# Kernel tuning notes

Hardware: AMD Instinct MI355X
Metric: run time of the kernel (lower is better)

The kernel has to match this reference:

```python
import jax, jax.numpy as jnp
import numpy as np

N = 100000
EPS_BN = 1e-5


def setup_inputs() -> dict:
    key = jax.random.key(0)
    ks = jax.random.split(key, 12)
    x = jax.random.normal(ks[0], (N, 128), dtype=jnp.float32)
    edge_index = jax.random.randint(ks[1], (2, 800000), 0, N, dtype=jnp.int64)
    # GCNConv layer params (PyG: lin weight [out,in], bias added after aggregation)
    s = 1.0 / np.sqrt(128.0)
    W1 = jax.random.uniform(ks[2], (128, 128), jnp.float32, -s, s)
    b1 = jnp.zeros((128,), jnp.float32)
    W2 = jax.random.uniform(ks[3], (128, 128), jnp.float32, -s, s)
    b2 = jnp.zeros((128,), jnp.float32)
    # BatchNorm affine params
    g1 = jnp.ones((128,), jnp.float32)
    be1 = jnp.zeros((128,), jnp.float32)
    g2 = jnp.ones((128,), jnp.float32)
    be2 = jnp.zeros((128,), jnp.float32)
    # PReLU single shared parameter (torch init = 0.25)
    a = jnp.asarray(0.25, jnp.float32)
    return {"x": x, "edge_index": edge_index, "W1": W1, "b1": b1, "g1": g1,
            "be1": be1, "W2": W2, "b2": b2, "g2": g2, "be2": be2, "a": a}


def _gcn_conv(x, src, dst, deg_inv_sqrt, W, b):
    # x' = D^-1/2 (A+I) D^-1/2 (x W^T) + b  (self loops already in src/dst)
    h = x @ W.T                                   # [N, out]
    norm = deg_inv_sqrt[src] * deg_inv_sqrt[dst]  # [E+N]
    msg = h[src] * norm[:, None]                  # gather + scale
    out = jax.ops.segment_sum(msg, dst, num_segments=N)  # scatter-add
    return out + b


def _batchnorm(x, g, be):
    # training-mode BatchNorm1d over nodes (biased variance)
    mean = jnp.mean(x, axis=0)
    var = jnp.mean(jnp.square(x - mean), axis=0)
    return (x - mean) * jax.lax.rsqrt(var + EPS_BN) * g + be


def _prelu(x, a):
    return jnp.where(x > 0, x, a * x)


def reference(x, edge_index, W1, b1, g1, be1, W2, b2, g2, be2, a):
    # add self loops
    loops = jnp.arange(N, dtype=edge_index.dtype)
    src = jnp.concatenate([edge_index[0], loops])
    dst = jnp.concatenate([edge_index[1], loops])
    # symmetric normalization from in-degree at destinations
    deg = jax.ops.segment_sum(jnp.ones_like(dst, dtype=x.dtype), dst, num_segments=N)
    deg_inv_sqrt = jnp.where(deg > 0, jax.lax.rsqrt(deg), 0.0)

    h = _gcn_conv(x, src, dst, deg_inv_sqrt, W1, b1)
    h = _prelu(_batchnorm(h, g1, be1), a)
    h = _gcn_conv(h, src, dst, deg_inv_sqrt, W2, b2)
    h = _prelu(_batchnorm(h, g2, be2), a)
    return h
```

## Files before the change

kernel.cpp:

```cpp
#include <hip/hip_runtime.h>
#include <cstddef>
#include <cstdint>


#define EPS_BN 1e-5f
#define BN_BLOCKS 256

typedef short short8 __attribute__((ext_vector_type(8)));
typedef float f32x4 __attribute__((ext_vector_type(4)));

static __device__ __forceinline__ unsigned short f2b(float f) {
    union { float f; uint32_t u; } v; v.f = f;
    uint32_t u = v.u;
    return (unsigned short)((u + 0x7FFFu + ((u >> 16) & 1u)) >> 16);
}
static __device__ __forceinline__ float b2f(unsigned short h) {
    union { uint32_t u; float f; } v; v.u = ((uint32_t)h) << 16;
    return v.f;
}
static __device__ __forceinline__ float b2f_s(short h) { return b2f((unsigned short)h); }

__global__ __launch_bounds__(256) void k_count(const int* __restrict__ dst, int* __restrict__ cnt,
                                               int* __restrict__ rank, int E) {
    int e = blockIdx.x * 256 + threadIdx.x;
    if (e < E) rank[e] = atomicAdd(&cnt[dst[e]], 1);
}

__global__ __launch_bounds__(256) void k_scanA(const int* __restrict__ cnt, int* __restrict__ partial, int n) {
    __shared__ int sd[256];
    int tid = threadIdx.x;
    int base = blockIdx.x * 1024 + tid * 4;
    int s = 0;
#pragma unroll
    for (int j = 0; j < 4; j++) { int idx = base + j; if (idx < n) s += cnt[idx]; }
    sd[tid] = s; __syncthreads();
    for (int off = 128; off > 0; off >>= 1) {
        if (tid < off) sd[tid] += sd[tid + off];
        __syncthreads();
    }
    if (tid == 0) partial[blockIdx.x] = sd[0];
}

__global__ __launch_bounds__(128) void k_scanB(int* partial, int nb) {
    __shared__ int sd[128];
    int t = threadIdx.x;
    sd[t] = (t < nb) ? partial[t] : 0;
    __syncthreads();
    for (int off = 1; off < 128; off <<= 1) {
        int v = (t >= off) ? sd[t - off] : 0;
        __syncthreads();
        sd[t] += v;
        __syncthreads();
    }
    if (t < nb) partial[t] = (t == 0) ? 0 : sd[t - 1];
}

__global__ __launch_bounds__(256) void k_scanC(const int* __restrict__ cnt, const int* __restrict__ partial,
                                               int* __restrict__ rowptr, float* __restrict__ dis, int n) {
    __shared__ int sd[256];
    int tid = threadIdx.x;
    int base = blockIdx.x * 1024 + tid * 4;
    int v[4]; int s = 0;
#pragma unroll
    for (int j = 0; j < 4; j++) { int idx = base + j; v[j] = (idx < n) ? cnt[idx] : 0; s += v[j]; }
    sd[tid] = s; __syncthreads();
    for (int off = 1; off < 256; off <<= 1) {
        int u = (tid >= off) ? sd[tid - off] : 0;
        __syncthreads();
        sd[tid] += u;
        __syncthreads();
    }
    int excl = partial[blockIdx.x] + ((tid == 0) ? 0 : sd[tid - 1]);
#pragma unroll
    for (int j = 0; j < 4; j++) {
        int idx = base + j;
        if (idx < n) {
            rowptr[idx] = excl;
            dis[idx] = rsqrtf((float)(v[j] + 1));
        }
        excl += v[j];
    }
}

__global__ __launch_bounds__(256) void k_fill(const int* __restrict__ src, const int* __restrict__ dst,
                                              const int* __restrict__ rowptr, const int* __restrict__ rank,
                                              int* __restrict__ colw, int E) {
    int e = blockIdx.x * 256 + threadIdx.x;
    if (e < E) {
        int d = dst[e];
        colw[rowptr[d] + rank[e]] = src[e];
    }
}

__global__ __launch_bounds__(256) void k_wprep(const float* __restrict__ W1, const float* __restrict__ W2,
                                               unsigned short* __restrict__ Wz1, unsigned short* __restrict__ Wz2) {
    int gi = blockIdx.x * 256 + threadIdx.x;
    const float* W = (gi < 16384) ? W1 : W2;
    unsigned short* Wz = (gi < 16384) ? Wz1 : Wz2;
    int idx = gi & 16383;
    int o = idx >> 7, k = idx & 127;
    int ct = o >> 4, nn = o & 15, ks = k >> 5, q = (k >> 3) & 3, j = k & 7;
    Wz[(ct * 4 + ks) * 512 + (q * 16 + nn) * 8 + j] = f2b(W[idx]);
}

__global__ __launch_bounds__(256) void k_gemm1(const float* __restrict__ X,
                                               const unsigned short* __restrict__ Wz,
                                               unsigned short* __restrict__ Yb, int n) {
    __shared__ unsigned short lds[16384];
    int tid = threadIdx.x;
    const short8* wsrc = (const short8*)Wz;
    short8* ldst = (short8*)lds;
#pragma unroll
    for (int i = 0; i < 8; i++) ldst[tid + 256 * i] = wsrc[tid + 256 * i];
    __syncthreads();

    int wave = tid >> 6, lane = tid & 63;
    int r0 = blockIdx.x * 64 + wave * 16;
    int mrow = lane & 15, quad = lane >> 4;
    int arow = r0 + mrow; if (arow > n - 1) arow = n - 1;
    const float* xr = X + (size_t)arow * 128;

    f32x4 acc[8];
#pragma unroll
    for (int ct = 0; ct < 8; ct++) acc[ct] = (f32x4){0.f, 0.f, 0.f, 0.f};

#pragma unroll
    for (int ks = 0; ks < 4; ks++) {
        int kb = ks * 32 + quad * 8;
        float4 x0 = *reinterpret_cast<const float4*>(xr + kb);
        float4 x1 = *reinterpret_cast<const float4*>(xr + kb + 4);
        short8 a;
        a[0] = (short)f2b(x0.x); a[1] = (short)f2b(x0.y); a[2] = (short)f2b(x0.z); a[3] = (short)f2b(x0.w);
        a[4] = (short)f2b(x1.x); a[5] = (short)f2b(x1.y); a[6] = (short)f2b(x1.z); a[7] = (short)f2b(x1.w);
#pragma unroll
        for (int ct = 0; ct < 8; ct++) {
            short8 b = *(const short8*)(lds + (ct * 4 + ks) * 512 + lane * 8);
            acc[ct] = __builtin_amdgcn_mfma_f32_16x16x32_bf16(a, b, acc[ct], 0, 0, 0);
        }
    }
#pragma unroll
    for (int i = 0; i < 4; i++) {
        int row = r0 + quad * 4 + i;
        if (row < n) {
#pragma unroll
            for (int ct = 0; ct < 8; ct++)
                Yb[(size_t)row * 128 + ct * 16 + mrow] = f2b(acc[ct][i]);
        }
    }
}

__global__ __launch_bounds__(256) void k_gemm2(const unsigned short* __restrict__ Ab,
                                               const unsigned short* __restrict__ Wz,
                                               const float* __restrict__ sc, const float* __restrict__ sh,
                                               const float* __restrict__ ap,
                                               unsigned short* __restrict__ Yb, int n) {
    __shared__ unsigned short lds[16384];
    int tid = threadIdx.x;
    const short8* wsrc = (const short8*)Wz;
    short8* ldst = (short8*)lds;
#pragma unroll
    for (int i = 0; i < 8; i++) ldst[tid + 256 * i] = wsrc[tid + 256 * i];
    __syncthreads();

    float alpha = ap[0];
    int wave = tid >> 6, lane = tid & 63;
    int r0 = blockIdx.x * 64 + wave * 16;
    int mrow = lane & 15, quad = lane >> 4;
    int arow = r0 + mrow; if (arow > n - 1) arow = n - 1;
    const unsigned short* ar = Ab + (size_t)arow * 128;

    f32x4 acc[8];
#pragma unroll
    for (int ct = 0; ct < 8; ct++) acc[ct] = (f32x4){0.f, 0.f, 0.f, 0.f};

#pragma unroll
    for (int ks = 0; ks < 4; ks++) {
        int kb = ks * 32 + quad * 8;
        short8 raw = *(const short8*)(ar + kb);
        float4 s0 = *reinterpret_cast<const float4*>(sc + kb);
        float4 s1 = *reinterpret_cast<const float4*>(sc + kb + 4);
        float4 t0 = *reinterpret_cast<const float4*>(sh + kb);
        float4 t1 = *reinterpret_cast<const float4*>(sh + kb + 4);
        float ss[8] = {s0.x, s0.y, s0.z, s0.w, s1.x, s1.y, s1.z, s1.w};
        float tt[8] = {t0.x, t0.y, t0.z, t0.w, t1.x, t1.y, t1.z, t1.w};
        short8 a;
#pragma unroll
        for (int j = 0; j < 8; j++) {
            float x = fmaf(b2f_s(raw[j]), ss[j], tt[j]);
            x = x > 0.f ? x : alpha * x;
            a[j] = (short)f2b(x);
        }
#pragma unroll
        for (int ct = 0; ct < 8; ct++) {
            short8 b = *(const short8*)(lds + (ct * 4 + ks) * 512 + lane * 8);
            acc[ct] = __builtin_amdgcn_mfma_f32_16x16x32_bf16(a, b, acc[ct], 0, 0, 0);
        }
    }
#pragma unroll
    for (int i = 0; i < 4; i++) {
        int row = r0 + quad * 4 + i;
        if (row < n) {
#pragma unroll
            for (int ct = 0; ct < 8; ct++)
                Yb[(size_t)row * 128 + ct * 16 + mrow] = f2b(acc[ct][i]);
        }
    }
}

__global__ __launch_bounds__(256) void k_agg(const unsigned short* __restrict__ Hb,
                                             const int* __restrict__ rowptr, const int* __restrict__ cnt,
                                             const int* __restrict__ colw, const float* __restrict__ dis,
                                             const float* __restrict__ bias,
                                             unsigned short* __restrict__ outb, int n) {
    int lane = threadIdx.x & 15;
    int node = blockIdx.x * 16 + (threadIdx.x >> 4);
    if (node >= n) return;
    int lo = lane * 8;
    float dn = dis[node];
    short8 hv = *(const short8*)(Hb + (size_t)node * 128 + lo);
    float acc[8];
#pragma unroll
    for (int j = 0; j < 8; j++) acc[j] = dn * b2f_s(hv[j]);
    int num = cnt[node];
    int beg = rowptr[node];
    const int* cw = colw + beg;
    int e = 0;
    for (; e + 4 <= num; e += 4) {
        int s0 = cw[e], s1 = cw[e + 1], s2 = cw[e + 2], s3 = cw[e + 3];
        float w0 = dis[s0], w1 = dis[s1], w2 = dis[s2], w3 = dis[s3];
        short8 n0 = *(const short8*)(Hb + (size_t)s0 * 128 + lo);
        short8 n1 = *(const short8*)(Hb + (size_t)s1 * 128 + lo);
        short8 n2 = *(const short8*)(Hb + (size_t)s2 * 128 + lo);
        short8 n3 = *(const short8*)(Hb + (size_t)s3 * 128 + lo);
#pragma unroll
        for (int j = 0; j < 8; j++) {
            acc[j] = fmaf(w0, b2f_s(n0[j]), acc[j]);
            acc[j] = fmaf(w1, b2f_s(n1[j]), acc[j]);
            acc[j] = fmaf(w2, b2f_s(n2[j]), acc[j]);
            acc[j] = fmaf(w3, b2f_s(n3[j]), acc[j]);
        }
    }
    for (; e < num; ++e) {
        int s = cw[e];
        float w = dis[s];
        short8 nb = *(const short8*)(Hb + (size_t)s * 128 + lo);
#pragma unroll
        for (int j = 0; j < 8; j++) acc[j] = fmaf(w, b2f_s(nb[j]), acc[j]);
    }
    const float4 bv0 = reinterpret_cast<const float4*>(bias)[lane * 2 + 0];
    const float4 bv1 = reinterpret_cast<const float4*>(bias)[lane * 2 + 1];
    float bb[8] = {bv0.x, bv0.y, bv0.z, bv0.w, bv1.x, bv1.y, bv1.z, bv1.w};
    short8 ov;
#pragma unroll
    for (int j = 0; j < 8; j++) ov[j] = (short)f2b(fmaf(dn, acc[j], bb[j]));
    *(short8*)(outb + (size_t)node * 128 + lo) = ov;
}

__global__ __launch_bounds__(256) void k_bnstats(const unsigned short* __restrict__ X, float* __restrict__ part, int n) {
    __shared__ float ls[16][128];
    __shared__ float lq[16][128];
    int tid = threadIdx.x;
    int rs = tid >> 4, g = tid & 15;
    float s[8], q[8];
#pragma unroll
    for (int j = 0; j < 8; j++) { s[j] = 0.f; q[j] = 0.f; }
#pragma unroll 4
    for (int r = blockIdx.x * 16 + rs; r < n; r += BN_BLOCKS * 16) {
        short8 v = *(const short8*)(X + (size_t)r * 128 + g * 8);
#pragma unroll
        for (int j = 0; j < 8; j++) {
            float f = b2f_s(v[j]);
            s[j] += f; q[j] = fmaf(f, f, q[j]);
        }
    }
#pragma unroll
    for (int j = 0; j < 8; j++) { ls[rs][g * 8 + j] = s[j]; lq[rs][g * 8 + j] = q[j]; }
    __syncthreads();
    for (int off = 8; off > 0; off >>= 1) {
        if (rs < off) {
#pragma unroll
            for (int j = 0; j < 8; j++) {
                ls[rs][g * 8 + j] += ls[rs + off][g * 8 + j];
                lq[rs][g * 8 + j] += lq[rs + off][g * 8 + j];
            }
        }
        __syncthreads();
    }
    if (tid < 128) part[blockIdx.x * 256 + tid] = ls[0][tid];
    else           part[blockIdx.x * 256 + tid] = lq[0][tid - 128];
}

__global__ __launch_bounds__(128) void k_bnparams(const float* __restrict__ part, const float* __restrict__ g,
                                                  const float* __restrict__ be, float* __restrict__ sc,
                                                  float* __restrict__ sh, float invN) {
    int f = threadIdx.x;
    float s = 0.f, q = 0.f;
#pragma unroll 8
    for (int b = 0; b < BN_BLOCKS; b++) {
        s += part[b * 256 + f];
        q += part[b * 256 + 128 + f];
    }
    float mean = s * invN;
    float var = q * invN - mean * mean;
    float rstd = rsqrtf(var + EPS_BN);
    float scale = g[f] * rstd;
    sc[f] = scale;
    sh[f] = fmaf(-mean, scale, be[f]);
}

__global__ __launch_bounds__(256) void k_bnact_f(const unsigned short* __restrict__ X, float* __restrict__ Y,
                                                 const float* __restrict__ sc, const float* __restrict__ sh,
                                                 const float* __restrict__ ap, int n8) {
    int i = blockIdx.x * 256 + threadIdx.x;
    if (i >= n8) return;
    float a = ap[0];
    int g = i & 15;
    const float4 s0 = reinterpret_cast<const float4*>(sc)[g * 2 + 0];
    const float4 s1 = reinterpret_cast<const float4*>(sc)[g * 2 + 1];
    const float4 t0 = reinterpret_cast<const float4*>(sh)[g * 2 + 0];
    const float4 t1 = reinterpret_cast<const float4*>(sh)[g * 2 + 1];
    float ss[8] = {s0.x, s0.y, s0.z, s0.w, s1.x, s1.y, s1.z, s1.w};
    float tt[8] = {t0.x, t0.y, t0.z, t0.w, t1.x, t1.y, t1.z, t1.w};
    short8 v = reinterpret_cast<const short8*>(X)[i];
    float out[8];
#pragma unroll
    for (int j = 0; j < 8; j++) {
        float x = fmaf(b2f_s(v[j]), ss[j], tt[j]);
        out[j] = x > 0.f ? x : a * x;
    }
    float4 o0 = {out[0], out[1], out[2], out[3]};
    float4 o1 = {out[4], out[5], out[6], out[7]};
    reinterpret_cast<float4*>(Y)[i * 2 + 0] = o0;
    reinterpret_cast<float4*>(Y)[i * 2 + 1] = o1;
}

extern "C" void kernel_launch(void* const* d_in, const int* in_sizes, int n_in,
                              void* d_out, int out_size, void* d_ws, size_t ws_size,
                              hipStream_t stream) {
    (void)n_in; (void)out_size; (void)ws_size;
    const float* x   = (const float*)d_in[0];
    const int*   ei  = (const int*)d_in[1];
    const float* W1  = (const float*)d_in[2];
    const float* b1  = (const float*)d_in[3];
    const float* g1  = (const float*)d_in[4];
    const float* be1 = (const float*)d_in[5];
    const float* W2  = (const float*)d_in[6];
    const float* b2  = (const float*)d_in[7];
    const float* g2  = (const float*)d_in[8];
    const float* be2 = (const float*)d_in[9];
    const float* ap  = (const float*)d_in[10];
    float* out = (float*)d_out;

    const int N = in_sizes[0] / 128;
    const int E = in_sizes[1] / 2;
    const int* srcIdx = ei;
    const int* dstIdx = ei + E;

    char* w = (char*)d_ws;
    size_t off = 0;
    auto alloc = [&](size_t bytes) { char* p = w + off; off += (bytes + 255) & ~(size_t)255; return p; };
    int*   cnt     = (int*)  alloc((size_t)N * 4);
    int*   rowptr  = (int*)  alloc((size_t)N * 4);
    int*   rank    = (int*)  alloc((size_t)E * 4);
    int*   colw    = (int*)  alloc((size_t)E * 4);
    float* dis     = (float*)alloc((size_t)N * 4);
    int*   partial = (int*)  alloc(4096);
    float* part    = (float*)alloc((size_t)BN_BLOCKS * 256 * 4);
    float* sc1     = (float*)alloc(512);
    float* sh1     = (float*)alloc(512);
    float* sc2     = (float*)alloc(512);
    float* sh2     = (float*)alloc(512);
    unsigned short* Wz1 = (unsigned short*)alloc(16384 * 2);
    unsigned short* Wz2 = (unsigned short*)alloc(16384 * 2);
    unsigned short* bufH = (unsigned short*)alloc((size_t)N * 128 * 2);
    unsigned short* bufA = (unsigned short*)alloc((size_t)N * 128 * 2);

    const float invN = 1.0f / (float)N;
    const int NB = (N + 1023) / 1024;
    const int gE = (E + 255) / 256;
    const int n8 = N * 16;
    const int gGemm = (N + 63) / 64;
    const int gAgg  = (N + 15) / 16;

    hipMemsetAsync(cnt, 0, (size_t)N * 4, stream);

    k_wprep<<<128, 256, 0, stream>>>(W1, W2, Wz1, Wz2);

    k_count<<<gE, 256, 0, stream>>>(dstIdx, cnt, rank, E);
    k_scanA<<<NB, 256, 0, stream>>>(cnt, partial, N);
    k_scanB<<<1, 128, 0, stream>>>(partial, NB);
    k_scanC<<<NB, 256, 0, stream>>>(cnt, partial, rowptr, dis, N);
    k_fill<<<gE, 256, 0, stream>>>(srcIdx, dstIdx, rowptr, rank, colw, E);

    k_gemm1<<<gGemm, 256, 0, stream>>>(x, Wz1, bufH, N);
    k_agg<<<gAgg, 256, 0, stream>>>(bufH, rowptr, cnt, colw, dis, b1, bufA, N);
    k_bnstats<<<BN_BLOCKS, 256, 0, stream>>>(bufA, part, N);
    k_bnparams<<<1, 128, 0, stream>>>(part, g1, be1, sc1, sh1, invN);

    k_gemm2<<<gGemm, 256, 0, stream>>>(bufA, Wz2, sc1, sh1, ap, bufH, N);
    k_agg<<<gAgg, 256, 0, stream>>>(bufH, rowptr, cnt, colw, dis, b2, bufA, N);
    k_bnstats<<<BN_BLOCKS, 256, 0, stream>>>(bufA, part, N);
    k_bnparams<<<1, 128, 0, stream>>>(part, g2, be2, sc2, sh2, invN);
    k_bnact_f<<<(n8 + 255) / 256, 256, 0, stream>>>(bufA, out, sc2, sh2, ap, n8);
}
```

Before: 318.3 us.

## Merge prep kernels, fold scanB into scanC, parallelize bnparams reduction

Fuses weight conversion with edge counting, fuses CSR fill with the first GEMM launch by adding extra blocks, removes the separate single-block scan kernel by having every scanC block redundantly scan the block partials, and widens bnparams to 1024 threads with an LDS reduction. The goal is fewer kernel launches and serial gaps on a launch-bound pipeline, plus a shorter single-block BN reduction. The risks are redundant partial scans in each scanC block and mixed block types sharing LDS allocation in the fused GEMM kernel. It relies on NB being at most 256.

```diff
diff --git a/kernel.cpp b/kernel.cpp
--- a/kernel.cpp
+++ b/kernel.cpp
@@ -20,10 +20,23 @@
 }
 static __device__ __forceinline__ float b2f_s(short h) { return b2f((unsigned short)h); }
 
-__global__ __launch_bounds__(256) void k_count(const int* __restrict__ dst, int* __restrict__ cnt,
-                                               int* __restrict__ rank, int E) {
-    int e = blockIdx.x * 256 + threadIdx.x;
-    if (e < E) rank[e] = atomicAdd(&cnt[dst[e]], 1);
+__global__ __launch_bounds__(256) void k_prep(const float* __restrict__ W1, const float* __restrict__ W2,
+                                              unsigned short* __restrict__ Wz1, unsigned short* __restrict__ Wz2,
+                                              const int* __restrict__ dst, int* __restrict__ cnt,
+                                              int* __restrict__ rank, int E) {
+    int bid = blockIdx.x, tid = threadIdx.x;
+    if (bid < 128) {
+        int gi = bid * 256 + tid;
+        const float* W = (gi < 16384) ? W1 : W2;
+        unsigned short* Wz = (gi < 16384) ? Wz1 : Wz2;
+        int idx = gi & 16383;
+        int o = idx >> 7, k = idx & 127;
+        int ct = o >> 4, nn = o & 15, ks = k >> 5, q = (k >> 3) & 3, j = k & 7;
+        Wz[(ct * 4 + ks) * 512 + (q * 16 + nn) * 8 + j] = f2b(W[idx]);
+    } else {
+        int e = (bid - 128) * 256 + tid;
+        if (e < E) rank[e] = atomicAdd(&cnt[dst[e]], 1);
+    }
 }
 
 __global__ __launch_bounds__(256) void k_scanA(const int* __restrict__ cnt, int* __restrict__ partial, int n) {
@@ -41,36 +54,27 @@
     if (tid == 0) partial[blockIdx.x] = sd[0];
 }
 
-__global__ __launch_bounds__(128) void k_scanB(int* partial, int nb) {
-    __shared__ int sd[128];
-    int t = threadIdx.x;
-    sd[t] = (t < nb) ? partial[t] : 0;
-    __syncthreads();
-    for (int off = 1; off < 128; off <<= 1) {
-        int v = (t >= off) ? sd[t - off] : 0;
-        __syncthreads();
-        sd[t] += v;
-        __syncthreads();
-    }
-    if (t < nb) partial[t] = (t == 0) ? 0 : sd[t - 1];
-}
-
 __global__ __launch_bounds__(256) void k_scanC(const int* __restrict__ cnt, const int* __restrict__ partial,
-                                               int* __restrict__ rowptr, float* __restrict__ dis, int n) {
+                                               int* __restrict__ rowptr, float* __restrict__ dis, int n, int nb) {
+    __shared__ int sp[256];
     __shared__ int sd[256];
     int tid = threadIdx.x;
+    sp[tid] = (tid < nb) ? partial[tid] : 0;
     int base = blockIdx.x * 1024 + tid * 4;
     int v[4]; int s = 0;
 #pragma unroll
     for (int j = 0; j < 4; j++) { int idx = base + j; v[j] = (idx < n) ? cnt[idx] : 0; s += v[j]; }
-    sd[tid] = s; __syncthreads();
+    sd[tid] = s;
+    __syncthreads();
     for (int off = 1; off < 256; off <<= 1) {
-        int u = (tid >= off) ? sd[tid - off] : 0;
+        int a = (tid >= off) ? sp[tid - off] : 0;
+        int b = (tid >= off) ? sd[tid - off] : 0;
         __syncthreads();
-        sd[tid] += u;
+        sp[tid] += a; sd[tid] += b;
         __syncthreads();
     }
-    int excl = partial[blockIdx.x] + ((tid == 0) ? 0 : sd[tid - 1]);
+    int gbase = (blockIdx.x == 0) ? 0 : sp[blockIdx.x - 1];
+    int excl = gbase + ((tid == 0) ? 0 : sd[tid - 1]);
 #pragma unroll
     for (int j = 0; j < 4; j++) {
         int idx = base + j;
@@ -82,32 +86,22 @@
     }
 }
 
-__global__ __launch_bounds__(256) void k_fill(const int* __restrict__ src, const int* __restrict__ dst,
-                                              const int* __restrict__ rowptr, const int* __restrict__ rank,
-                                              int* __restrict__ colw, int E) {
-    int e = blockIdx.x * 256 + threadIdx.x;
-    if (e < E) {
-        int d = dst[e];
-        colw[rowptr[d] + rank[e]] = src[e];
-    }
-}
-
-__global__ __launch_bounds__(256) void k_wprep(const float* __restrict__ W1, const float* __restrict__ W2,
-                                               unsigned short* __restrict__ Wz1, unsigned short* __restrict__ Wz2) {
-    int gi = blockIdx.x * 256 + threadIdx.x;
-    const float* W = (gi < 16384) ? W1 : W2;
-    unsigned short* Wz = (gi < 16384) ? Wz1 : Wz2;
-    int idx = gi & 16383;
-    int o = idx >> 7, k = idx & 127;
-    int ct = o >> 4, nn = o & 15, ks = k >> 5, q = (k >> 3) & 3, j = k & 7;
-    Wz[(ct * 4 + ks) * 512 + (q * 16 + nn) * 8 + j] = f2b(W[idx]);
-}
-
-__global__ __launch_bounds__(256) void k_gemm1(const float* __restrict__ X,
-                                               const unsigned short* __restrict__ Wz,
-                                               unsigned short* __restrict__ Yb, int n) {
+__global__ __launch_bounds__(256) void k_fill_gemm1(const float* __restrict__ X,
+                                                    const unsigned short* __restrict__ Wz,
+                                                    unsigned short* __restrict__ Yb, int n,
+                                                    const int* __restrict__ src, const int* __restrict__ dst,
+                                                    const int* __restrict__ rowptr, const int* __restrict__ rank,
+                                                    int* __restrict__ colw, int E, int gGemm) {
     __shared__ unsigned short lds[16384];
     int tid = threadIdx.x;
+    if ((int)blockIdx.x >= gGemm) {
+        int e = (blockIdx.x - gGemm) * 256 + tid;
+        if (e < E) {
+            int d = dst[e];
+            colw[rowptr[d] + rank[e]] = src[e];
+        }
+        return;
+    }
     const short8* wsrc = (const short8*)Wz;
     short8* ldst = (short8*)lds;
 #pragma unroll
@@ -290,22 +284,32 @@
     else           part[blockIdx.x * 256 + tid] = lq[0][tid - 128];
 }
 
-__global__ __launch_bounds__(128) void k_bnparams(const float* __restrict__ part, const float* __restrict__ g,
-                                                  const float* __restrict__ be, float* __restrict__ sc,
-                                                  float* __restrict__ sh, float invN) {
-    int f = threadIdx.x;
+__global__ __launch_bounds__(1024) void k_bnparams(const float* __restrict__ part, const float* __restrict__ g,
+                                                   const float* __restrict__ be, float* __restrict__ sc,
+                                                   float* __restrict__ sh, float invN) {
+    __shared__ float lsum[8][128];
+    __shared__ float lsq[8][128];
+    int tid = threadIdx.x;
+    int f = tid & 127, c = tid >> 7;
     float s = 0.f, q = 0.f;
-#pragma unroll 8
-    for (int b = 0; b < BN_BLOCKS; b++) {
+#pragma unroll 4
+    for (int b = c * 32; b < c * 32 + 32; b++) {
         s += part[b * 256 + f];
         q += part[b * 256 + 128 + f];
     }
-    float mean = s * invN;
-    float var = q * invN - mean * mean;
-    float rstd = rsqrtf(var + EPS_BN);
-    float scale = g[f] * rstd;
-    sc[f] = scale;
-    sh[f] = fmaf(-mean, scale, be[f]);
+    lsum[c][f] = s; lsq[c][f] = q;
+    __syncthreads();
+    if (tid < 128) {
+        float ss = 0.f, qq = 0.f;
+#pragma unroll
+        for (int c2 = 0; c2 < 8; c2++) { ss += lsum[c2][tid]; qq += lsq[c2][tid]; }
+        float mean = ss * invN;
+        float var = qq * invN - mean * mean;
+        float rstd = rsqrtf(var + EPS_BN);
+        float scale = g[tid] * rstd;
+        sc[tid] = scale;
+        sh[tid] = fmaf(-mean, scale, be[tid]);
+    }
 }
 
 __global__ __launch_bounds__(256) void k_bnact_f(const unsigned short* __restrict__ X, float* __restrict__ Y,
@@ -384,22 +388,20 @@
 
     hipMemsetAsync(cnt, 0, (size_t)N * 4, stream);
 
-    k_wprep<<<128, 256, 0, stream>>>(W1, W2, Wz1, Wz2);
-
-    k_count<<<gE, 256, 0, stream>>>(dstIdx, cnt, rank, E);
+    k_prep<<<128 + gE, 256, 0, stream>>>(W1, W2, Wz1, Wz2, dstIdx, cnt, rank, E);
+
     k_scanA<<<NB, 256, 0, stream>>>(cnt, partial, N);
-    k_scanB<<<1, 128, 0, stream>>>(partial, NB);
-    k_scanC<<<NB, 256, 0, stream>>>(cnt, partial, rowptr, dis, N);
-    k_fill<<<gE, 256, 0, stream>>>(srcIdx, dstIdx, rowptr, rank, colw, E);
-
-    k_gemm1<<<gGemm, 256, 0, stream>>>(x, Wz1, bufH, N);
+    k_scanC<<<NB, 256, 0, stream>>>(cnt, partial, rowptr, dis, N, NB);
+
+    k_fill_gemm1<<<gGemm + gE, 256, 0, stream>>>(x, Wz1, bufH, N,
+                                                 srcIdx, dstIdx, rowptr, rank, colw, E, gGemm);
     k_agg<<<gAgg, 256, 0, stream>>>(bufH, rowptr, cnt, colw, dis, b1, bufA, N);
     k_bnstats<<<BN_BLOCKS, 256, 0, stream>>>(bufA, part, N);
-    k_bnparams<<<1, 128, 0, stream>>>(part, g1, be1, sc1, sh1, invN);
+    k_bnparams<<<1, 1024, 0, stream>>>(part, g1, be1, sc1, sh1, invN);
 
     k_gemm2<<<gGemm, 256, 0, stream>>>(bufA, Wz2, sc1, sh1, ap, bufH, N);
     k_agg<<<gAgg, 256, 0, stream>>>(bufH, rowptr, cnt, colw, dis, b2, bufA, N);
     k_bnstats<<<BN_BLOCKS, 256, 0, stream>>>(bufA, part, N);
-    k_bnparams<<<1, 128, 0, stream>>>(part, g2, be2, sc2, sh2, invN);
+    k_bnparams<<<1, 1024, 0, stream>>>(part, g2, be2, sc2, sh2, invN);
     k_bnact_f<<<(n8 + 255) / 256, 256, 0, stream>>>(bufA, out, sc2, sh2, ap, n8);
 }
```

After: 296.7 us. 1.07x faster.
